# Kernel optimization log

Hardware: AMD Instinct MI355X
Metric: run time of the kernel (lower is better)

The kernel has to match this reference:

```python
import jax, jax.numpy as jnp
import numpy as np

N_HEADS = 16
LN_EPS = 1e-5

def _layernorm(x, g, b):
    m = jnp.mean(x, axis=-1, keepdims=True)
    v = jnp.var(x, axis=-1, keepdims=True)
    return (x - m) * jax.lax.rsqrt(v + LN_EPS) * g + b

def setup_inputs() -> dict:
    key = jax.random.key(0)
    ks = jax.random.split(key, 6)
    B, L, D = 4, 1024, 1024
    Dff = 4 * D
    s = 0.02  # init scale to keep logits/activations in a sane range
    return {
        "X": jax.random.normal(ks[0], (B, L, D), jnp.float32),
        "wq": jax.random.normal(ks[1], (D, D), jnp.float32) * s,
        "wk": jax.random.normal(ks[2], (D, D), jnp.float32) * s,
        "wv": jax.random.normal(ks[3], (D, D), jnp.float32) * s,
        "ln1_g": jnp.ones((D,), jnp.float32),
        "ln1_b": jnp.zeros((D,), jnp.float32),
        "w1": jax.random.normal(ks[4], (Dff, D), jnp.float32) * s,
        "b1": jnp.zeros((Dff,), jnp.float32),
        "w2": jax.random.normal(ks[5], (D, Dff), jnp.float32) * s,
        "b2": jnp.zeros((D,), jnp.float32),
        "ln2_g": jnp.ones((D,), jnp.float32),
        "ln2_b": jnp.zeros((D,), jnp.float32),
    }

def reference(X, wq, wk, wv, ln1_g, ln1_b, w1, b1, w2, b2, ln2_g, ln2_b):
    B, L, D = X.shape
    H = N_HEADS
    dh = D // H
    # qkv projections (torch Linear: x @ W^T), split into heads
    Q = (X @ wq.T).reshape(B, L, H, dh)
    K = (X @ wk.T).reshape(B, L, H, dh)
    V = (X @ wv.T).reshape(B, L, H, dh)
    scores = jnp.einsum("blhd,bmhd->bhlm", Q, K)  # [B,H,L,L]
    causal = jnp.tril(jnp.ones((L, L), dtype=bool))
    scores = jnp.where(causal, scores, -jnp.inf)
    attn = jax.nn.softmax(scores / jnp.sqrt(jnp.asarray(dh, X.dtype)), axis=-1)
    ctx = jnp.einsum("bhlm,bmhd->blhd", attn, V).reshape(B, L, D)
    # post-LN residual (note: no output projection after attention)
    X = _layernorm(X + ctx, ln1_g, ln1_b)
    h = jax.nn.selu(X @ w1.T + b1)
    X = _layernorm(X + h @ w2.T + b2, ln2_g, ln2_b)
    return X
```

## Files before the change

### kernel.cpp

```cpp
#include <hip/hip_runtime.h>
#include <hip/hip_bf16.h>

#define BATCH 4
#define SEQ   1024
#define DIM   1024
#define NH    16
#define DH    64
#define DFF   4096
#define MTOK  (BATCH*SEQ)

#define QSCALE 0.1803368801111204f

typedef __attribute__((ext_vector_type(8))) short  short8;
typedef __attribute__((ext_vector_type(4))) short  short4v;
typedef __attribute__((ext_vector_type(4))) float  floatx4;
typedef __attribute__((ext_vector_type(4))) float  float4v;
typedef __attribute__((ext_vector_type(4))) int    int4v;

__device__ inline float bf2f(short s) {
    return __uint_as_float(((unsigned int)(unsigned short)s) << 16);
}
__device__ inline short f2bf(float f) {
    __hip_bfloat16 h = __float2bfloat16(f);
    return *reinterpret_cast<short*>(&h);
}

__device__ inline float wave_sum(float v) {
    #pragma unroll
    for (int off = 32; off >= 1; off >>= 1) v += __shfl_xor(v, off);
    return v;
}

__device__ inline void async_ld16(short* lds, const short* g) {
    __builtin_amdgcn_global_load_lds(
        (const __attribute__((address_space(1))) void*)g,
        (__attribute__((address_space(3))) void*)lds, 16, 0, 0);
}

__global__ __launch_bounds__(256) void convert_all(
    const float* __restrict__ sX,  short* __restrict__ dX,
    const float* __restrict__ sq,  short* __restrict__ dq,
    const float* __restrict__ sk,  short* __restrict__ dk,
    const float* __restrict__ sv,  short* __restrict__ dv,
    const float* __restrict__ s1,  short* __restrict__ d1,
    const float* __restrict__ s2,  short* __restrict__ d2)
{
    int cid = blockIdx.x * 256 + threadIdx.x;
    const float* src; short* dst; int base;
    if      (cid <  524288) { src = sX; dst = dX; base = 0; }
    else if (cid <  655360) { src = sq; dst = dq; base = 524288; }
    else if (cid <  786432) { src = sk; dst = dk; base = 655360; }
    else if (cid <  917504) { src = sv; dst = dv; base = 786432; }
    else if (cid < 1441792) { src = s1; dst = d1; base = 917504; }
    else                    { src = s2; dst = d2; base = 1441792; }
    size_t i = (size_t)(cid - base) * 8;
    float4v f0 = *(const float4v*)(src + i);
    float4v f1 = *(const float4v*)(src + i + 4);
    short8 o;
    o[0]=f2bf(f0[0]); o[1]=f2bf(f0[1]); o[2]=f2bf(f0[2]); o[3]=f2bf(f0[3]);
    o[4]=f2bf(f1[0]); o[5]=f2bf(f1[1]); o[6]=f2bf(f1[2]); o[7]=f2bf(f1[3]);
    *(short8*)(dst + i) = o;
}

template<int EPI>
__global__ __launch_bounds__(256, 2) void gemm128d(
    const short* __restrict__ A, const short* __restrict__ B,
    const float* __restrict__ bias, short* __restrict__ C, int N, int K)
{
    __shared__ __align__(16) short Ls[32768];

    const int t    = threadIdx.x;
    const int lane = t & 63;
    const int wave = t >> 6;
    const int quad = lane >> 4;
    const int l15  = lane & 15;
    const int wm   = wave & 1;
    const int wn   = wave >> 1;
    const int tm   = blockIdx.x * 128;
    const int tn   = blockIdx.y * 128;

    int kbase = 0, klen = K;
    if (EPI == 3) { klen = K >> 2; kbase = blockIdx.z * klen; }
    const int NT = klen >> 6;

    const int g8 = (((t & 7) ^ ((t >> 3) & 7)) << 3);
    int offR[4];
    #pragma unroll
    for (int i = 0; i < 4; i++) offR[i] = (i*32 + (t >> 3)) * K + g8;
    const short* Abase = A + (size_t)tm * K + kbase;
    const short* Bbase = B + (size_t)tn * K + kbase;
    short* dstb = &Ls[t * 8];

    const int xa  = (wm*64 + l15) * 64;
    const int xb  = (wn*64 + l15) * 64;
    const int sw  = l15 & 7;
    const int xc0 = ((quad ^ sw) << 3);
    const int xc1 = (((4 + quad) ^ sw) << 3);

    short8 a[4][2], b[4][2];
    floatx4 acc[4][4];
    #pragma unroll
    for (int mt = 0; mt < 4; mt++)
        #pragma unroll
        for (int nt = 0; nt < 4; nt++) acc[mt][nt] = {0.f, 0.f, 0.f, 0.f};

#define STAGE_TILE(buf, k0) do { _Pragma("unroll")                    \
    for (int _i = 0; _i < 4; _i++) {                                  \
        async_ld16(dstb + (buf)*16384 + _i*2048,        Abase + offR[_i] + (k0)); \
        async_ld16(dstb + (buf)*16384 + 8192 + _i*2048, Bbase + offR[_i] + (k0)); \
    } } while (0)

#define LDAB(buf) do { _Pragma("unroll")                              \
    for (int _mt = 0; _mt < 4; _mt++) {                               \
        a[_mt][0] = *(const short8*)&Ls[(buf)*16384 + xa + _mt*1024 + xc0]; \
        a[_mt][1] = *(const short8*)&Ls[(buf)*16384 + xa + _mt*1024 + xc1]; \
        b[_mt][0] = *(const short8*)&Ls[(buf)*16384 + 8192 + xb + _mt*1024 + xc0]; \
        b[_mt][1] = *(const short8*)&Ls[(buf)*16384 + 8192 + xb + _mt*1024 + xc1]; \
    } } while (0)

#define MM32() do { __builtin_amdgcn_s_setprio(1); _Pragma("unroll")  \
    for (int _c = 0; _c < 2; _c++) { _Pragma("unroll")                \
        for (int _mt = 0; _mt < 4; _mt++) { _Pragma("unroll")         \
            for (int _nn = 0; _nn < 4; _nn++) {                       \
                acc[_mt][_nn] = __builtin_amdgcn_mfma_f32_16x16x32_bf16( \
                    a[_mt][_c], b[_nn][_c], acc[_mt][_nn], 0, 0, 0);  \
            } } }                                                     \
    __builtin_amdgcn_s_setprio(0); } while (0)

    STAGE_TILE(0, 0);
    __syncthreads();

    for (int kt = 0; kt < NT; ++kt) {
        const int cur = kt & 1;
        if (kt + 1 < NT) STAGE_TILE(cur ^ 1, (kt + 1) << 6);
        LDAB(cur);
        MM32();
        __syncthreads();
    }

    const float SS = 1.0507009873554805f;
    const float SA = 1.6732632423543772f;

    #pragma unroll
    for (int mt = 0; mt < 4; mt++) {
        int row0 = tm + wm*64 + mt*16 + quad*4;
        #pragma unroll
        for (int nt = 0; nt < 4; nt++) {
            int col = tn + wn*64 + nt*16 + l15;
            if (EPI == 0 && (col >> 10) == 2) {
                int h = (col >> 6) & 15, d = col & 63;
                int bb = row0 >> 10, key = row0 & 1023;
                short4v pv;
                #pragma unroll
                for (int r = 0; r < 4; r++) pv[r] = f2bf(acc[mt][nt][r]);
                *(short4v*)&C[(size_t)2*MTOK*1024
                    + ((size_t)(bb*16 + h)*64 + d)*1024 + key] = pv;
                continue;
            }
            #pragma unroll
            for (int r = 0; r < 4; r++) {
                int row = row0 + r;
                float v = acc[mt][nt][r];
                if (EPI == 0) {
                    int which = col >> 10;
                    if (which == 0) v *= QSCALE;
                    C[(size_t)which * ((size_t)MTOK*1024)
                      + (size_t)row * 1024 + (col & 1023)] = f2bf(v);
                } else if (EPI == 1) {
                    v += bias[col];
                    v = (v > 0.f) ? SS * v
                                  : SS * SA * (exp2f(v * 1.44269504f) - 1.f);
                    C[(size_t)row * N + col] = f2bf(v);
                } else {
                    C[(size_t)blockIdx.z * ((size_t)MTOK*N)
                      + (size_t)row * N + col] = f2bf(v);
                }
            }
        }
    }
#undef STAGE_TILE
#undef LDAB
#undef MM32
}

__global__ __launch_bounds__(256) void attn_kernel(
    const short* __restrict__ Q, const short* __restrict__ K,
    const short* __restrict__ Vt, short* __restrict__ CTX)
{
    __shared__ __align__(16) short Ks[2][64*64];
    __shared__ __align__(16) short Vs[2][64*64];
    __shared__ __align__(16) short Pl[4][32][72];

    const int t    = threadIdx.x;
    const int lane = t & 63;
    const int wave = t >> 6;
    const int quad = lane >> 4;
    const int l15  = lane & 15;
    const int q0 = (gridDim.x - 1 - blockIdx.x) * 128;
    const int bh = blockIdx.y;
    const int b  = bh >> 4;
    const int h  = bh & 15;

    const size_t headoff = (size_t)b * SEQ * DIM + (size_t)h * DH;
    const short* Qb  = Q + headoff;
    const short* Kb  = K + headoff;
    const short* Vtb = Vt + (size_t)bh * DH * SEQ;

    const int wrow0 = q0 + wave*32;

    short8 aq[2][2];
    #pragma unroll
    for (int mg = 0; mg < 2; mg++)
        #pragma unroll
        for (int c = 0; c < 2; c++)
            aq[mg][c] = *(const short8*)(Qb
                + (size_t)(wrow0 + mg*16 + l15) * DIM + c*32 + quad*8);

    short8 bones;
    {
        short v = (l15 == 0) ? (short)0x3F80 : (short)0;
        #pragma unroll
        for (int e = 0; e < 8; e++) bones[e] = v;
    }

    floatx4 o[2][4], ol[2];
    #pragma unroll
    for (int mg = 0; mg < 2; mg++) {
        #pragma unroll
        for (int nt = 0; nt < 4; nt++) o[mg][nt] = {0.f, 0.f, 0.f, 0.f};
        ol[mg] = {0.f, 0.f, 0.f, 0.f};
    }

    const int swz = (((t & 7) ^ ((t >> 3) & 7))) * 8;
    auto stage = [&](int j0, int sb) {
        #pragma unroll
        for (int p = 0; p < 2; p++) {
            async_ld16(Ks[sb] + (t + p*256)*8,
                       Kb + (size_t)(j0 + (t>>3) + p*32) * DIM + swz);
            async_ld16(Vs[sb] + (t + p*256)*8,
                       Vtb + (size_t)((t>>3) + p*32) * SEQ + j0 + swz);
        }
    };

    const int jend = q0 + 128;
    stage(0, 0);
    __syncthreads();

    int sb = 0;
    for (int j0 = 0; j0 < jend; j0 += 64) {
        if (j0 + 64 < jend) stage(j0 + 64, sb ^ 1);

        if (j0 <= wrow0 + 31) {
            floatx4 s[2][4];
            #pragma unroll
            for (int mg = 0; mg < 2; mg++)
                #pragma unroll
                for (int nt = 0; nt < 4; nt++) s[mg][nt] = {0.f, 0.f, 0.f, 0.f};
            #pragma unroll
            for (int c = 0; c < 2; c++) {
                #pragma unroll
                for (int nt = 0; nt < 4; nt++) {
                    short8 bk = *(const short8*)&Ks[sb][(nt*16 + l15)*64
                                  + ((c*4 + quad) ^ (l15 & 7))*8];
                    s[0][nt] = __builtin_amdgcn_mfma_f32_16x16x32_bf16(bk, aq[0][c], s[0][nt], 0, 0, 0);
                    s[1][nt] = __builtin_amdgcn_mfma_f32_16x16x32_bf16(bk, aq[1][c], s[1][nt], 0, 0, 0);
                }
            }

            if (j0 + 63 > wrow0) {
                #pragma unroll
                for (int mg = 0; mg < 2; mg++) {
                    int rowq = wrow0 + mg*16 + l15;
                    #pragma unroll
                    for (int nt = 0; nt < 4; nt++) {
                        #pragma unroll
                        for (int r = 0; r < 4; r++) {
                            int key = j0 + nt*16 + quad*4 + r;
                            if (key > rowq) s[mg][nt][r] = -1.0e38f;
                        }
                    }
                }
            }

            #pragma unroll
            for (int mg = 0; mg < 2; mg++)
                #pragma unroll
                for (int nt = 0; nt < 4; nt++) {
                    short4v pv;
                    #pragma unroll
                    for (int r = 0; r < 4; r++)
                        pv[r] = f2bf(exp2f(s[mg][nt][r]));
                    *(short4v*)&Pl[wave][mg*16 + l15][nt*16 + quad*4] = pv;
                }

            #pragma unroll
            for (int c = 0; c < 2; c++) {
                short8 ap0 = *(const short8*)&Pl[wave][l15][c*32 + quad*8];
                short8 ap1 = *(const short8*)&Pl[wave][16 + l15][c*32 + quad*8];
                #pragma unroll
                for (int nt = 0; nt < 4; nt++) {
                    short8 bv = *(const short8*)&Vs[sb][(nt*16 + l15)*64
                                  + ((c*4 + quad) ^ (l15 & 7))*8];
                    o[0][nt] = __builtin_amdgcn_mfma_f32_16x16x32_bf16(ap0, bv, o[0][nt], 0, 0, 0);
                    o[1][nt] = __builtin_amdgcn_mfma_f32_16x16x32_bf16(ap1, bv, o[1][nt], 0, 0, 0);
                }
                ol[0] = __builtin_amdgcn_mfma_f32_16x16x32_bf16(ap0, bones, ol[0], 0, 0, 0);
                ol[1] = __builtin_amdgcn_mfma_f32_16x16x32_bf16(ap1, bones, ol[1], 0, 0, 0);
            }
        }

        __syncthreads();
        sb ^= 1;
    }

    #pragma unroll
    for (int mg = 0; mg < 2; mg++) {
        float linv[4];
        #pragma unroll
        for (int r = 0; r < 4; r++)
            linv[r] = 1.f / __shfl(ol[mg][r], lane & 48);
        #pragma unroll
        for (int nt = 0; nt < 4; nt++) {
            #pragma unroll
            for (int r = 0; r < 4; r++) {
                int rowq = wrow0 + mg*16 + quad*4 + r;
                int d    = nt*16 + l15;
                CTX[(size_t)b * SEQ * DIM + (size_t)rowq * DIM + h*DH + d]
                    = f2bf(o[mg][nt][r] * linv[r]);
            }
        }
    }
}

__global__ __launch_bounds__(256) void ln1_kernel(
    const float* __restrict__ X, const short* __restrict__ ctx,
    const float* __restrict__ g, const float* __restrict__ bvec,
    short* __restrict__ out)
{
    __shared__ float red[8];
    const size_t base = (size_t)blockIdx.x * DIM;
    const int wave = threadIdx.x >> 6;

    float x[4];
    float sum = 0.f, sq = 0.f;
    #pragma unroll
    for (int i = 0; i < 4; i++) {
        int idx = threadIdx.x + i*256;
        float v = X[base + idx] + bf2f(ctx[base + idx]);
        x[i] = v; sum += v; sq += v*v;
    }
    sum = wave_sum(sum); sq = wave_sum(sq);
    if ((threadIdx.x & 63) == 0) { red[wave] = sum; red[4 + wave] = sq; }
    __syncthreads();
    float s1 = red[0] + red[1] + red[2] + red[3];
    float s2 = red[4] + red[5] + red[6] + red[7];
    float mean = s1 * (1.f / DIM);
    float var  = s2 * (1.f / DIM) - mean * mean;
    float rstd = rsqrtf(var + 1e-5f);
    #pragma unroll
    for (int i = 0; i < 4; i++) {
        int idx = threadIdx.x + i*256;
        out[base + idx] = f2bf((x[i] - mean) * rstd * g[idx] + bvec[idx]);
    }
}

__global__ __launch_bounds__(256) void ln2_fused(
    const short* __restrict__ P, const float* __restrict__ bias,
    const short* __restrict__ x1, const float* __restrict__ g,
    const float* __restrict__ bvec, float* __restrict__ out)
{
    __shared__ float red[8];
    const size_t base = (size_t)blockIdx.x * DIM;
    const size_t E4 = (size_t)MTOK * 1024;
    const int wave = threadIdx.x >> 6;

    float x[4];
    float sum = 0.f, sq = 0.f;
    #pragma unroll
    for (int i = 0; i < 4; i++) {
        int idx = threadIdx.x + i*256;
        size_t p = base + idx;
        float v = bf2f(P[p]) + bf2f(P[E4 + p]) + bf2f(P[2*E4 + p])
                + bf2f(P[3*E4 + p]) + bias[idx] + bf2f(x1[p]);
        x[i] = v; sum += v; sq += v*v;
    }
    sum = wave_sum(sum); sq = wave_sum(sq);
    if ((threadIdx.x & 63) == 0) { red[wave] = sum; red[4 + wave] = sq; }
    __syncthreads();
    float s1 = red[0] + red[1] + red[2] + red[3];
    float s2 = red[4] + red[5] + red[6] + red[7];
    float mean = s1 * (1.f / DIM);
    float var  = s2 * (1.f / DIM) - mean * mean;
    float rstd = rsqrtf(var + 1e-5f);
    #pragma unroll
    for (int i = 0; i < 4; i++) {
        int idx = threadIdx.x + i*256;
        out[base + idx] = (x[i] - mean) * rstd * g[idx] + bvec[idx];
    }
}

extern "C" void kernel_launch(void* const* d_in, const int* in_sizes, int n_in,
                              void* d_out, int out_size, void* d_ws, size_t ws_size,
                              hipStream_t stream)
{
    const float* X   = (const float*)d_in[0];
    const float* wq  = (const float*)d_in[1];
    const float* wk  = (const float*)d_in[2];
    const float* wv  = (const float*)d_in[3];
    const float* g1  = (const float*)d_in[4];
    const float* b1  = (const float*)d_in[5];
    const float* w1  = (const float*)d_in[6];
    const float* bb1 = (const float*)d_in[7];
    const float* w2  = (const float*)d_in[8];
    const float* bb2 = (const float*)d_in[9];
    const float* g2  = (const float*)d_in[10];
    const float* b2  = (const float*)d_in[11];

    short* ws = (short*)d_ws;
    const size_t E1 = 1048576, E4 = 4194304;
    size_t o = 0;
    short* Xb    = ws + o; o += E4;
    short* wqkvb = ws + o; o += 3*E1;
    short* w1b   = ws + o; o += E4;
    short* w2b   = ws + o; o += E4;
    short* Q     = ws + o; o += E4;
    short* Kb    = ws + o; o += E4;
    short* Vt    = ws + o; o += E4;
    short* CTX   = ws + o; o += E4;
    short* X1    = ws + o; o += E4;
    short* P     = ws + o; o += 4*E4;
    short* Hf    = Q;

    dim3 blk(256);
    convert_all<<<dim3(7680), blk, 0, stream>>>(
        X, Xb, wq, wqkvb, wk, wqkvb + E1, wv, wqkvb + 2*E1,
        w1, w1b, w2, w2b);

    gemm128d<0><<<dim3(MTOK/128, 3072/128), blk, 0, stream>>>(
        Xb, wqkvb, nullptr, Q, 3072, DIM);
    attn_kernel<<<dim3(SEQ/128, BATCH*NH), blk, 0, stream>>>(Q, Kb, Vt, CTX);
    ln1_kernel<<<dim3(MTOK), blk, 0, stream>>>(X, CTX, g1, b1, X1);
    gemm128d<1><<<dim3(MTOK/128, DFF/128), blk, 0, stream>>>(
        X1, w1b, bb1, Hf, DFF, DIM);
    gemm128d<3><<<dim3(MTOK/128, DIM/128, 4), blk, 0, stream>>>(
        Hf, w2b, nullptr, P, DIM, DFF);
    ln2_fused<<<dim3(MTOK), blk, 0, stream>>>(P, bb2, X1, g2, b2, (float*)d_out);
}
```

Before: 278.5 us.

## Use 32x32x16 MFMA in GEMMs and halve attention query tile to 64

```diff
diff --git a/kernel.cpp b/kernel.cpp
--- a/kernel.cpp
+++ b/kernel.cpp
@@ -14,6 +14,7 @@
 typedef __attribute__((ext_vector_type(8))) short  short8;
 typedef __attribute__((ext_vector_type(4))) short  short4v;
 typedef __attribute__((ext_vector_type(4))) float  floatx4;
+typedef __attribute__((ext_vector_type(16))) float floatx16;
 typedef __attribute__((ext_vector_type(4))) float  float4v;
 typedef __attribute__((ext_vector_type(4))) int    int4v;
 
@@ -72,8 +73,8 @@
     const int t    = threadIdx.x;
     const int lane = t & 63;
     const int wave = t >> 6;
-    const int quad = lane >> 4;
-    const int l15  = lane & 15;
+    const int l31  = lane & 31;
+    const int hi   = lane >> 5;
     const int wm   = wave & 1;
     const int wn   = wave >> 1;
     const int tm   = blockIdx.x * 128;
@@ -91,18 +92,21 @@
     const short* Bbase = B + (size_t)tn * K + kbase;
     short* dstb = &Ls[t * 8];
 
-    const int xa  = (wm*64 + l15) * 64;
-    const int xb  = (wn*64 + l15) * 64;
-    const int sw  = l15 & 7;
-    const int xc0 = ((quad ^ sw) << 3);
-    const int xc1 = (((4 + quad) ^ sw) << 3);
-
-    short8 a[4][2], b[4][2];
-    floatx4 acc[4][4];
-    #pragma unroll
-    for (int mt = 0; mt < 4; mt++)
+    const int rowA = (wm*64 + l31) * 64;
+    const int rowB = 8192 + (wn*64 + l31) * 64;
+    int xg[4];
+    #pragma unroll
+    for (int ks = 0; ks < 4; ks++)
+        xg[ks] = (((ks*2 + hi) ^ (l31 & 7)) << 3);
+
+    short8 a[2][4], b[2][4];
+    floatx16 acc[2][2];
+    #pragma unroll
+    for (int mt = 0; mt < 2; mt++)
         #pragma unroll
-        for (int nt = 0; nt < 4; nt++) acc[mt][nt] = {0.f, 0.f, 0.f, 0.f};
+        for (int nt = 0; nt < 2; nt++)
+            #pragma unroll
+            for (int e = 0; e < 16; e++) acc[mt][nt][e] = 0.f;
 
 #define STAGE_TILE(buf, k0) do { _Pragma("unroll")                    \
     for (int _i = 0; _i < 4; _i++) {                                  \
@@ -111,19 +115,18 @@
     } } while (0)
 
 #define LDAB(buf) do { _Pragma("unroll")                              \
-    for (int _mt = 0; _mt < 4; _mt++) {                               \
-        a[_mt][0] = *(const short8*)&Ls[(buf)*16384 + xa + _mt*1024 + xc0]; \
-        a[_mt][1] = *(const short8*)&Ls[(buf)*16384 + xa + _mt*1024 + xc1]; \
-        b[_mt][0] = *(const short8*)&Ls[(buf)*16384 + 8192 + xb + _mt*1024 + xc0]; \
-        b[_mt][1] = *(const short8*)&Ls[(buf)*16384 + 8192 + xb + _mt*1024 + xc1]; \
-    } } while (0)
-
-#define MM32() do { __builtin_amdgcn_s_setprio(1); _Pragma("unroll")  \
-    for (int _c = 0; _c < 2; _c++) { _Pragma("unroll")                \
-        for (int _mt = 0; _mt < 4; _mt++) { _Pragma("unroll")         \
-            for (int _nn = 0; _nn < 4; _nn++) {                       \
-                acc[_mt][_nn] = __builtin_amdgcn_mfma_f32_16x16x32_bf16( \
-                    a[_mt][_c], b[_nn][_c], acc[_mt][_nn], 0, 0, 0);  \
+    for (int _mt = 0; _mt < 2; _mt++) { _Pragma("unroll")             \
+        for (int _ks = 0; _ks < 4; _ks++) {                           \
+            a[_mt][_ks] = *(const short8*)&Ls[(buf)*16384 + rowA + _mt*2048 + xg[_ks]]; \
+            b[_mt][_ks] = *(const short8*)&Ls[(buf)*16384 + rowB + _mt*2048 + xg[_ks]]; \
+        } } } while (0)
+
+#define MM16() do { __builtin_amdgcn_s_setprio(1); _Pragma("unroll")  \
+    for (int _ks = 0; _ks < 4; _ks++) { _Pragma("unroll")             \
+        for (int _mt = 0; _mt < 2; _mt++) { _Pragma("unroll")         \
+            for (int _nn = 0; _nn < 2; _nn++) {                       \
+                acc[_mt][_nn] = __builtin_amdgcn_mfma_f32_32x32x16_bf16( \
+                    a[_mt][_ks], b[_nn][_ks], acc[_mt][_nn], 0, 0, 0); \
             } } }                                                     \
     __builtin_amdgcn_s_setprio(0); } while (0)
 
@@ -134,7 +137,7 @@
         const int cur = kt & 1;
         if (kt + 1 < NT) STAGE_TILE(cur ^ 1, (kt + 1) << 6);
         LDAB(cur);
-        MM32();
+        MM16();
         __syncthreads();
     }
 
@@ -142,45 +145,52 @@
     const float SA = 1.6732632423543772f;
 
     #pragma unroll
-    for (int mt = 0; mt < 4; mt++) {
-        int row0 = tm + wm*64 + mt*16 + quad*4;
+    for (int mt = 0; mt < 2; mt++) {
+        int rbase = tm + wm*64 + mt*32 + hi*4;
         #pragma unroll
-        for (int nt = 0; nt < 4; nt++) {
-            int col = tn + wn*64 + nt*16 + l15;
+        for (int nt = 0; nt < 2; nt++) {
+            int col = tn + wn*64 + nt*32 + l31;
             if (EPI == 0 && (col >> 10) == 2) {
                 int h = (col >> 6) & 15, d = col & 63;
-                int bb = row0 >> 10, key = row0 & 1023;
-                short4v pv;
-                #pragma unroll
-                for (int r = 0; r < 4; r++) pv[r] = f2bf(acc[mt][nt][r]);
-                *(short4v*)&C[(size_t)2*MTOK*1024
-                    + ((size_t)(bb*16 + h)*64 + d)*1024 + key] = pv;
+                #pragma unroll
+                for (int g = 0; g < 4; g++) {
+                    int row0 = rbase + g*8;
+                    int bb = row0 >> 10, key = row0 & 1023;
+                    short4v pv;
+                    #pragma unroll
+                    for (int r = 0; r < 4; r++) pv[r] = f2bf(acc[mt][nt][g*4 + r]);
+                    *(short4v*)&C[(size_t)2*MTOK*1024
+                        + ((size_t)(bb*16 + h)*64 + d)*1024 + key] = pv;
+                }
                 continue;
             }
             #pragma unroll
-            for (int r = 0; r < 4; r++) {
-                int row = row0 + r;
-                float v = acc[mt][nt][r];
-                if (EPI == 0) {
-                    int which = col >> 10;
-                    if (which == 0) v *= QSCALE;
-                    C[(size_t)which * ((size_t)MTOK*1024)
-                      + (size_t)row * 1024 + (col & 1023)] = f2bf(v);
-                } else if (EPI == 1) {
-                    v += bias[col];
-                    v = (v > 0.f) ? SS * v
-                                  : SS * SA * (exp2f(v * 1.44269504f) - 1.f);
-                    C[(size_t)row * N + col] = f2bf(v);
-                } else {
-                    C[(size_t)blockIdx.z * ((size_t)MTOK*N)
-                      + (size_t)row * N + col] = f2bf(v);
+            for (int g = 0; g < 4; g++) {
+                #pragma unroll
+                for (int r = 0; r < 4; r++) {
+                    int row = rbase + g*8 + r;
+                    float v = acc[mt][nt][g*4 + r];
+                    if (EPI == 0) {
+                        int which = col >> 10;
+                        if (which == 0) v *= QSCALE;
+                        C[(size_t)which * ((size_t)MTOK*1024)
+                          + (size_t)row * 1024 + (col & 1023)] = f2bf(v);
+                    } else if (EPI == 1) {
+                        v += bias[col];
+                        v = (v > 0.f) ? SS * v
+                                      : SS * SA * (exp2f(v * 1.44269504f) - 1.f);
+                        C[(size_t)row * N + col] = f2bf(v);
+                    } else {
+                        C[(size_t)blockIdx.z * ((size_t)MTOK*N)
+                          + (size_t)row * N + col] = f2bf(v);
+                    }
                 }
             }
         }
     }
 #undef STAGE_TILE
 #undef LDAB
-#undef MM32
+#undef MM16
 }
 
 __global__ __launch_bounds__(256) void attn_kernel(
@@ -189,14 +199,14 @@
 {
     __shared__ __align__(16) short Ks[2][64*64];
     __shared__ __align__(16) short Vs[2][64*64];
-    __shared__ __align__(16) short Pl[4][32][72];
+    __shared__ __align__(16) short Pl[4][16][72];
 
     const int t    = threadIdx.x;
     const int lane = t & 63;
     const int wave = t >> 6;
     const int quad = lane >> 4;
     const int l15  = lane & 15;
-    const int q0 = (gridDim.x - 1 - blockIdx.x) * 128;
+    const int q0 = (gridDim.x - 1 - blockIdx.x) * 64;
     const int bh = blockIdx.y;
     const int b  = bh >> 4;
     const int h  = bh & 15;
@@ -206,15 +216,13 @@
     const short* Kb  = K + headoff;
     const short* Vtb = Vt + (size_t)bh * DH * SEQ;
 
-    const int wrow0 = q0 + wave*32;
-
-    short8 aq[2][2];
-    #pragma unroll
-    for (int mg = 0; mg < 2; mg++)
-        #pragma unroll
-        for (int c = 0; c < 2; c++)
-            aq[mg][c] = *(const short8*)(Qb
-                + (size_t)(wrow0 + mg*16 + l15) * DIM + c*32 + quad*8);
+    const int wrow0 = q0 + wave*16;
+
+    short8 aq[2];
+    #pragma unroll
+    for (int c = 0; c < 2; c++)
+        aq[c] = *(const short8*)(Qb
+            + (size_t)(wrow0 + l15) * DIM + c*32 + quad*8);
 
     short8 bones;
     {
@@ -223,13 +231,10 @@
         for (int e = 0; e < 8; e++) bones[e] = v;
     }
 
-    floatx4 o[2][4], ol[2];
-    #pragma unroll
-    for (int mg = 0; mg < 2; mg++) {
-        #pragma unroll
-        for (int nt = 0; nt < 4; nt++) o[mg][nt] = {0.f, 0.f, 0.f, 0.f};
-        ol[mg] = {0.f, 0.f, 0.f, 0.f};
-    }
+    floatx4 o[4], ol;
+    #pragma unroll
+    for (int nt = 0; nt < 4; nt++) o[nt] = {0.f, 0.f, 0.f, 0.f};
+    ol = {0.f, 0.f, 0.f, 0.f};
 
     const int swz = (((t & 7) ^ ((t >> 3) & 7))) * 8;
     auto stage = [&](int j0, int sb) {
@@ -242,7 +247,7 @@
         }
     };
 
-    const int jend = q0 + 128;
+    const int jend = q0 + 64;
     stage(0, 0);
     __syncthreads();
 
@@ -250,62 +255,51 @@
     for (int j0 = 0; j0 < jend; j0 += 64) {
         if (j0 + 64 < jend) stage(j0 + 64, sb ^ 1);
 
-        if (j0 <= wrow0 + 31) {
-            floatx4 s[2][4];
-            #pragma unroll
-            for (int mg = 0; mg < 2; mg++)
-                #pragma unroll
-                for (int nt = 0; nt < 4; nt++) s[mg][nt] = {0.f, 0.f, 0.f, 0.f};
+        if (j0 <= wrow0 + 15) {
+            floatx4 s[4];
+            #pragma unroll
+            for (int nt = 0; nt < 4; nt++) s[nt] = {0.f, 0.f, 0.f, 0.f};
             #pragma unroll
             for (int c = 0; c < 2; c++) {
                 #pragma unroll
                 for (int nt = 0; nt < 4; nt++) {
                     short8 bk = *(const short8*)&Ks[sb][(nt*16 + l15)*64
                                   + ((c*4 + quad) ^ (l15 & 7))*8];
-                    s[0][nt] = __builtin_amdgcn_mfma_f32_16x16x32_bf16(bk, aq[0][c], s[0][nt], 0, 0, 0);
-                    s[1][nt] = __builtin_amdgcn_mfma_f32_16x16x32_bf16(bk, aq[1][c], s[1][nt], 0, 0, 0);
+                    s[nt] = __builtin_amdgcn_mfma_f32_16x16x32_bf16(bk, aq[c], s[nt], 0, 0, 0);
                 }
             }
 
             if (j0 + 63 > wrow0) {
-                #pragma unroll
-                for (int mg = 0; mg < 2; mg++) {
-                    int rowq = wrow0 + mg*16 + l15;
+                int rowq = wrow0 + l15;
+                #pragma unroll
+                for (int nt = 0; nt < 4; nt++) {
                     #pragma unroll
-                    for (int nt = 0; nt < 4; nt++) {
-                        #pragma unroll
-                        for (int r = 0; r < 4; r++) {
-                            int key = j0 + nt*16 + quad*4 + r;
-                            if (key > rowq) s[mg][nt][r] = -1.0e38f;
-                        }
+                    for (int r = 0; r < 4; r++) {
+                        int key = j0 + nt*16 + quad*4 + r;
+                        if (key > rowq) s[nt][r] = -1.0e38f;
                     }
                 }
             }
 
             #pragma unroll
-            for (int mg = 0; mg < 2; mg++)
-                #pragma unroll
-                for (int nt = 0; nt < 4; nt++) {
-                    short4v pv;
-                    #pragma unroll
-                    for (int r = 0; r < 4; r++)
-                        pv[r] = f2bf(exp2f(s[mg][nt][r]));
-                    *(short4v*)&Pl[wave][mg*16 + l15][nt*16 + quad*4] = pv;
-                }
+            for (int nt = 0; nt < 4; nt++) {
+                short4v pv;
+                #pragma unroll
+                for (int r = 0; r < 4; r++)
+                    pv[r] = f2bf(exp2f(s[nt][r]));
+                *(short4v*)&Pl[wave][l15][nt*16 + quad*4] = pv;
+            }
 
             #pragma unroll
             for (int c = 0; c < 2; c++) {
-                short8 ap0 = *(const short8*)&Pl[wave][l15][c*32 + quad*8];
-                short8 ap1 = *(const short8*)&Pl[wave][16 + l15][c*32 + quad*8];
+                short8 ap = *(const short8*)&Pl[wave][l15][c*32 + quad*8];
                 #pragma unroll
                 for (int nt = 0; nt < 4; nt++) {
                     short8 bv = *(const short8*)&Vs[sb][(nt*16 + l15)*64
                                   + ((c*4 + quad) ^ (l15 & 7))*8];
-                    o[0][nt] = __builtin_amdgcn_mfma_f32_16x16x32_bf16(ap0, bv, o[0][nt], 0, 0, 0);
-                    o[1][nt] = __builtin_amdgcn_mfma_f32_16x16x32_bf16(ap1, bv, o[1][nt], 0, 0, 0);
+                    o[nt] = __builtin_amdgcn_mfma_f32_16x16x32_bf16(ap, bv, o[nt], 0, 0, 0);
                 }
-                ol[0] = __builtin_amdgcn_mfma_f32_16x16x32_bf16(ap0, bones, ol[0], 0, 0, 0);
-                ol[1] = __builtin_amdgcn_mfma_f32_16x16x32_bf16(ap1, bones, ol[1], 0, 0, 0);
+                ol = __builtin_amdgcn_mfma_f32_16x16x32_bf16(ap, bones, ol, 0, 0, 0);
             }
         }
 
@@ -313,21 +307,18 @@
         sb ^= 1;
     }
 
-    #pragma unroll
-    for (int mg = 0; mg < 2; mg++) {
-        float linv[4];
+    float linv[4];
+    #pragma unroll
+    for (int r = 0; r < 4; r++)
+        linv[r] = 1.f / __shfl(ol[r], lane & 48);
+    #pragma unroll
+    for (int nt = 0; nt < 4; nt++) {
         #pragma unroll
-        for (int r = 0; r < 4; r++)
-            linv[r] = 1.f / __shfl(ol[mg][r], lane & 48);
-        #pragma unroll
-        for (int nt = 0; nt < 4; nt++) {
-            #pragma unroll
-            for (int r = 0; r < 4; r++) {
-                int rowq = wrow0 + mg*16 + quad*4 + r;
-                int d    = nt*16 + l15;
-                CTX[(size_t)b * SEQ * DIM + (size_t)rowq * DIM + h*DH + d]
-                    = f2bf(o[mg][nt][r] * linv[r]);
-            }
+        for (int r = 0; r < 4; r++) {
+            int rowq = wrow0 + quad*4 + r;
+            int d    = nt*16 + l15;
+            CTX[(size_t)b * SEQ * DIM + (size_t)rowq * DIM + h*DH + d]
+                = f2bf(o[nt][r] * linv[r]);
         }
     }
 }
@@ -438,7 +429,7 @@
 
     gemm128d<0><<<dim3(MTOK/128, 3072/128), blk, 0, stream>>>(
         Xb, wqkvb, nullptr, Q, 3072, DIM);
-    attn_kernel<<<dim3(SEQ/128, BATCH*NH), blk, 0, stream>>>(Q, Kb, Vt, CTX);
+    attn_kernel<<<dim3(SEQ/64, BATCH*NH), blk, 0, stream>>>(Q, Kb, Vt, CTX);
     ln1_kernel<<<dim3(MTOK), blk, 0, stream>>>(X, CTX, g1, b1, X1);
     gemm128d<1><<<dim3(MTOK/128, DFF/128), blk, 0, stream>>>(
         X1, w1b, bb1, Hf, DFF, DIM);
```

New measurement: 300.7 us. 1.08x slower.
